# Optimization experiments

Measured on AMD Instinct MI355X. Metric: run time of the kernel, lower is better.

The kernel has to match this reference:

```python
import jax, jax.numpy as jnp
import numpy as np

N, F, E, WID, M, K = 100000, 128, 128, 4, 25000, 16
HID = WID * F    # width * num_features = 512
DHID = WID * E   # discriminator hidden = 512
EPS = 1e-5


def _v2v(x, v_idx, w_e):
    """Hypergraph v2v mean aggregation: v->e mean (scaled by w_e), then e->v mean."""
    Mm, Kk = v_idx.shape
    C = x.shape[1]
    ef = jnp.zeros((Mm, C), x.dtype)
    for k in range(Kk):  # K is small and static; avoids a [M,K,C] materialization
        ef = ef + x[v_idx[:, k]]
    ef = ef * (w_e / Kk)[:, None]  # weighted edge features [M, C]
    out = jnp.zeros_like(x)
    deg = jnp.zeros((x.shape[0],), x.dtype)
    for k in range(Kk):
        out = out.at[v_idx[:, k]].add(ef)
        deg = deg.at[v_idx[:, k]].add(1.0)
    return out / jnp.maximum(deg, 1.0)[:, None]


def _bn(h, g, bt):
    # BatchNorm1d in training mode: biased batch stats over vertex dim
    m = h.mean(0)
    v = ((h - m) ** 2).mean(0)
    return g * (h - m) * jax.lax.rsqrt(v + EPS) + bt


def _conv(x, Wt, b, g, bt, v_idx, w_e, last=False):
    h = _bn(x @ Wt.T + b, g, bt)
    h = _v2v(h, v_idx, w_e)
    return h if last else jax.nn.relu(h)  # dropout = identity (eval mode)


def setup_inputs() -> dict:
    key = jax.random.key(0)
    ks = iter(jax.random.split(key, 64))

    def lin(o, i):
        s = 1.0 / np.sqrt(i)
        return (jax.random.uniform(next(ks), (o, i), minval=-s, maxval=s, dtype=jnp.float32),
                jax.random.uniform(next(ks), (o,), minval=-s, maxval=s, dtype=jnp.float32))

    d = {}
    d["X"] = jax.random.normal(next(ks), (N, F), dtype=jnp.float32)
    d["v_idx"] = jax.random.randint(next(ks), (M, K), 0, N, dtype=jnp.int32)
    d["w_e"] = jax.random.uniform(next(ks), (M,), dtype=jnp.float32)
    for name, (o, i) in [("enc1", (HID, F)), ("enc2", (E, HID)), ("fc", (E, HID)),
                         ("f1u", (E, E)), ("f2u", (E, E)), ("f1r", (E, E)), ("f2r", (E, E)),
                         ("f1", (E, E)), ("f2", (E, E)),
                         ("dis1", (DHID, E)), ("dis2", (2, DHID)),
                         ("dec1", (HID, E)), ("dec2", (F, HID))]:
        Wt, b = lin(o, i)
        d[name + "_W"] = Wt
        d[name + "_b"] = b
    for name, c in [("enc1", HID), ("enc2", E), ("dis1", DHID), ("dis2", 2), ("dec1", HID), ("dec2", F)]:
        d[name + "_g"] = jnp.ones((c,), jnp.float32)
        d[name + "_bt"] = jnp.zeros((c,), jnp.float32)
    return d


def reference(X, v_idx, w_e,
              enc1_W, enc1_b, enc2_W, enc2_b, fc_W, fc_b,
              f1u_W, f1u_b, f2u_W, f2u_b, f1r_W, f1r_b, f2r_W, f2r_b,
              f1_W, f1_b, f2_W, f2_b,
              dis1_W, dis1_b, dis2_W, dis2_b, dec1_W, dec1_b, dec2_W, dec2_b,
              enc1_g, enc1_bt, enc2_g, enc2_bt, dis1_g, dis1_bt, dis2_g, dis2_bt,
              dec1_g, dec1_bt, dec2_g, dec2_bt):
    # encoder (returns last output and first-layer output)
    x1 = _conv(X, enc1_W, enc1_b, enc1_g, enc1_bt, v_idx, w_e)            # [N, HID]
    xe = _conv(x1, enc2_W, enc2_b, enc2_g, enc2_bt, v_idx, w_e, last=True)  # [N, E]
    xe1 = x1 @ fc_W.T + fc_b                                               # [N, E]
    # GRU-style gating
    z = jax.nn.sigmoid(xe1 @ f1u_W.T + f1u_b + xe @ f2u_W.T + f2u_b)
    r = jax.nn.sigmoid(xe1 @ f1r_W.T + f1r_b + xe @ f2r_W.T + f2r_b)
    o = jnp.tanh(xe1 @ f1_W.T + f1_b + (r * xe) @ f2_W.T + f2_b)
    outs = z * o + (1.0 - z) * xe                                          # [N, E]
    # attention pooling (n = input_size - 1)
    dd = (outs - outs.mean(0)) ** 2
    vv = dd.sum(0) / (N - 1)
    ee = dd / (4.0 * (vv + 0.001)) + 0.5
    proto = (outs * jax.nn.sigmoid(ee)).sum(0)                             # [E]
    # gradient reversal is identity in the forward pass
    h = _conv(outs, dis1_W, dis1_b, dis1_g, dis1_bt, v_idx, w_e)
    xdis = _conv(h, dis2_W, dis2_b, dis2_g, dis2_bt, v_idx, w_e, last=True)  # [N, 2]
    h = _conv(outs, dec1_W, dec1_b, dec1_g, dec1_bt, v_idx, w_e)
    x_de = _conv(h, dec2_W, dec2_b, dec2_g, dec2_bt, v_idx, w_e, last=True)  # [N, F]
    return (outs, x_de, proto, xdis)
```

## Files before the change

### kernel.cpp

```cpp
#include <hip/hip_runtime.h>
#include <cstddef>
#include <cstdint>

static constexpr int NV = 100000;
static constexpr int NP = 100096;
static constexpr int ME = 25000;
static constexpr int MEP = 25088;
static constexpr int KE = 16;
static constexpr float BN_EPS = 1e-5f;

typedef unsigned int u32;
typedef __attribute__((ext_vector_type(8))) short s16x8;
typedef __attribute__((ext_vector_type(8))) unsigned short u16x8;
typedef __attribute__((ext_vector_type(4))) float f32x4;

__device__ __forceinline__ float sigm(float x) { return 1.0f / (1.0f + expf(-x)); }
__device__ __forceinline__ float bf2f(unsigned short u) {
    union { u32 i; float f; } v; v.i = ((u32)u) << 16; return v.f;
}
__device__ __forceinline__ unsigned short f2bf(float f) {
    union { float f; u32 i; } v; v.f = f;
    u32 u = v.i;
    return (unsigned short)((u + 0x7FFFu + ((u >> 16) & 1u)) >> 16);
}

#define GLD16(g, l) __builtin_amdgcn_global_load_lds(                          \
    (__attribute__((address_space(1))) const unsigned int*)(g),                \
    (__attribute__((address_space(3))) unsigned int*)(l), 16, 0, 0)

__global__ __launch_bounds__(256)
void mfma_gemm(const unsigned short* __restrict__ A, int IC,
               const unsigned short* __restrict__ W, const float* __restrict__ bias,
               unsigned short* __restrict__ Cb, int ldb, int cb0,
               unsigned short* __restrict__ Cb2, int ldb2, int splitN,
               float* __restrict__ s1f, float* __restrict__ s2f, int statsC)
{
    __shared__ unsigned short smA[128 * 64];
    const int bm = blockIdx.y * 128;
    const int bn = blockIdx.x * 64;
    const int tid = threadIdx.x;
    const int l = tid & 63, w = tid >> 6;
    const int wrow = w >> 1, wcol = w & 1;

    f32x4 acc[4][2];
    #pragma unroll
    for (int m = 0; m < 4; ++m)
        #pragma unroll
        for (int n = 0; n < 2; ++n)
            #pragma unroll
            for (int r = 0; r < 4; ++r) acc[m][n][r] = 0.f;

    const int swz = (((l & 7) ^ (l >> 3)) << 3);

    for (int k0 = 0; k0 < IC; k0 += 64) {
        #pragma unroll
        for (int i = 0; i < 4; ++i) {
            const unsigned short* g = A + (size_t)(bm + 32 * w + 8 * i + (l >> 3)) * IC + k0 + swz;
            GLD16(g, smA + 2048 * w + 512 * i);
        }
        s16x8 bfr[2][2];
        #pragma unroll
        for (int n = 0; n < 2; ++n)
            #pragma unroll
            for (int ks = 0; ks < 2; ++ks) {
                int col = bn + wcol * 32 + n * 16 + (l & 15);
                bfr[n][ks] = *(const s16x8*)&W[(size_t)col * IC + k0 + ks * 32 + ((l >> 4) << 3)];
            }
        __syncthreads();
        #pragma unroll
        for (int ks = 0; ks < 2; ++ks) {
            s16x8 afr[4];
            #pragma unroll
            for (int m = 0; m < 4; ++m) {
                int row = wrow * 64 + m * 16 + (l & 15);
                int off = row * 64 + ((ks * 32 + ((l >> 4) << 3)) ^ ((l & 7) << 3));
                afr[m] = *(const s16x8*)&smA[off];
            }
            #pragma unroll
            for (int m = 0; m < 4; ++m)
                #pragma unroll
                for (int n = 0; n < 2; ++n)
                    acc[m][n] = __builtin_amdgcn_mfma_f32_16x16x32_bf16(
                        afr[m], bfr[n][ks], acc[m][n], 0, 0, 0);
        }
        __syncthreads();
    }

    unsigned short* dst = Cb;
    int ld = ldb, co = cb0;
    if (Cb2 && bn >= splitN) { dst = Cb2; ld = ldb2; co = -splitN; }

    #pragma unroll
    for (int n = 0; n < 2; ++n) {
        const int col = bn + wcol * 32 + n * 16 + (l & 15);
        const float bs = bias[col];
        float ssum = 0.f, sq = 0.f;
        #pragma unroll
        for (int m = 0; m < 4; ++m) {
            const int row0 = bm + wrow * 64 + m * 16 + ((l >> 4) << 2);
            #pragma unroll
            for (int r = 0; r < 4; ++r) {
                float v = acc[m][n][r] + bs;
                int row = row0 + r;
                if (dst) dst[(size_t)row * ld + co + col] = f2bf(v);
                if (s1f && col < statsC && row < NV) { ssum += v; sq += v * v; }
            }
        }
        if (s1f && col < statsC) {
            ssum += __shfl_xor(ssum, 16); ssum += __shfl_xor(ssum, 32);
            sq   += __shfl_xor(sq, 16);   sq   += __shfl_xor(sq, 32);
            if ((l >> 4) == 0) {
                atomicAdd(&s1f[col], ssum);
                atomicAdd(&s2f[col], sq);
            }
        }
    }
}

__global__ __launch_bounds__(256)
void mfma_gemm_ef(const unsigned short* __restrict__ A,
                  const unsigned short* __restrict__ W,
                  const float* __restrict__ we,
                  const float* __restrict__ P, const float* __restrict__ Q,
                  unsigned short* __restrict__ ef, int ldE)
{
    __shared__ unsigned short smA[128 * 64];
    const int bm = blockIdx.y * 128;
    const int bn = blockIdx.x * 64;
    const int tid = threadIdx.x;
    const int l = tid & 63, w = tid >> 6;
    const int wrow = w >> 1, wcol = w & 1;

    f32x4 acc[4][2];
    #pragma unroll
    for (int m = 0; m < 4; ++m)
        #pragma unroll
        for (int n = 0; n < 2; ++n)
            #pragma unroll
            for (int r = 0; r < 4; ++r) acc[m][n][r] = 0.f;

    const int swz = (((l & 7) ^ (l >> 3)) << 3);

    for (int k0 = 0; k0 < 128; k0 += 64) {
        #pragma unroll
        for (int i = 0; i < 4; ++i) {
            const unsigned short* g = A + (size_t)(bm + 32 * w + 8 * i + (l >> 3)) * 128 + k0 + swz;
            GLD16(g, smA + 2048 * w + 512 * i);
        }
        s16x8 bfr[2][2];
        #pragma unroll
        for (int n = 0; n < 2; ++n)
            #pragma unroll
            for (int ks = 0; ks < 2; ++ks) {
                int col = bn + wcol * 32 + n * 16 + (l & 15);
                bfr[n][ks] = *(const s16x8*)&W[(size_t)col * 128 + k0 + ks * 32 + ((l >> 4) << 3)];
            }
        __syncthreads();
        #pragma unroll
        for (int ks = 0; ks < 2; ++ks) {
            s16x8 afr[4];
            #pragma unroll
            for (int m = 0; m < 4; ++m) {
                int row = wrow * 64 + m * 16 + (l & 15);
                int off = row * 64 + ((ks * 32 + ((l >> 4) << 3)) ^ ((l & 7) << 3));
                afr[m] = *(const s16x8*)&smA[off];
            }
            #pragma unroll
            for (int m = 0; m < 4; ++m)
                #pragma unroll
                for (int n = 0; n < 2; ++n)
                    acc[m][n] = __builtin_amdgcn_mfma_f32_16x16x32_bf16(
                        afr[m], bfr[n][ks], acc[m][n], 0, 0, 0);
        }
        __syncthreads();
    }

    #pragma unroll
    for (int n = 0; n < 2; ++n) {
        const int col = bn + wcol * 32 + n * 16 + (l & 15);
        const float pc = P[col], qc = Q[col];
        #pragma unroll
        for (int m = 0; m < 4; ++m) {
            const int row0 = bm + wrow * 64 + m * 16 + ((l >> 4) << 2);
            #pragma unroll
            for (int r = 0; r < 4; ++r) {
                int row = row0 + r;
                if (row < ME) {
                    float wv = we[row];
                    ef[(size_t)row * ldE + col] = f2bf(wv * (pc * acc[m][n][r] + qc));
                }
            }
        }
    }
}

__global__ void prep_weights(const float* e1, const float* e2, const float* fcw,
                             const float* d1, const float* dc1, const float* dc2,
                             const float* ds2,
                             const float* f1u, const float* f2u,
                             const float* f1r, const float* f2r,
                             const float* f1, const float* f2,
                             const float* f1ub, const float* f2ub,
                             const float* f1rb, const float* f2rb,
                             const float* f1b, const float* f2b,
                             const float* ds1b, const float* dc1b,
                             const float* e2b, const float* fcb,
                             unsigned short* WB, float* bzr, float* bo,
                             float* bdd, float* bef)
{
    int i = blockIdx.x * 256 + threadIdx.x;
    if (i < 65536)           WB[i] = f2bf(e1[i]);
    else if (i < 131072)     WB[i] = f2bf(e2[i - 65536]);
    else if (i < 196608)     WB[i] = f2bf(fcw[i - 131072]);
    else if (i < 262144)     WB[i] = f2bf(d1[i - 196608]);
    else if (i < 327680)     WB[i] = f2bf(dc1[i - 262144]);
    else if (i < 393216)     WB[i] = f2bf(dc2[i - 327680]);
    else if (i < 394240)     WB[i] = f2bf(ds2[i - 393216]);
    else if (i < 459776) {
        int j = i - 394240, row = j >> 8, c = j & 255;
        float v;
        if (row < 128) v = (c < 128) ? f1u[row * 128 + c] : f2u[row * 128 + c - 128];
        else { int rr = row - 128; v = (c < 128) ? f1r[rr * 128 + c] : f2r[rr * 128 + c - 128]; }
        WB[i] = f2bf(v);
    } else if (i < 492544) {
        int j = i - 459776, row = j >> 8, c = j & 255;
        float v = (c < 128) ? f1[row * 128 + c] : f2[row * 128 + c - 128];
        WB[i] = f2bf(v);
    } else if (i < 492800) {
        int o = i - 492544;
        bzr[o] = (o < 128) ? (f1ub[o] + f2ub[o]) : (f1rb[o - 128] + f2rb[o - 128]);
    } else if (i < 492928) {
        int o = i - 492800;
        bo[o] = f1b[o] + f2b[o];
    } else if (i < 493952) {
        int o = i - 492928;
        bdd[o] = (o < 512) ? ds1b[o] : dc1b[o - 512];
    } else if (i < 494208) {
        int o = i - 493952;
        bef[o] = (o < 128) ? e2b[o] : fcb[o - 128];
    }
}

__global__ void cvt_f32_bf16(const float* __restrict__ in, unsigned short* __restrict__ out, int n)
{
    int i = (blockIdx.x * 256 + threadIdx.x) * 4;
    if (i < n) {
        float4 v = *reinterpret_cast<const float4*>(&in[i]);
        out[i] = f2bf(v.x); out[i + 1] = f2bf(v.y);
        out[i + 2] = f2bf(v.z); out[i + 3] = f2bf(v.w);
    }
}

__global__ void bn_finalize_kernel(const float* __restrict__ s1, const float* __restrict__ s2,
                                   const float* __restrict__ g, const float* __restrict__ bt,
                                   float* __restrict__ scale, float* __restrict__ shift,
                                   int C, float invN)
{
    int c = threadIdx.x;
    if (c < C) {
        float m = s1[c] * invN;
        float v = fmaxf(s2[c] * invN - m * m, 0.f);
        float sc = g[c] * rsqrtf(v + BN_EPS);
        scale[c] = sc;
        shift[c] = bt[c] - m * sc;
    }
}

__global__ void bn_finalize_pq(const float* __restrict__ s1, const float* __restrict__ s2,
                               const float* __restrict__ g, const float* __restrict__ bt,
                               const float* __restrict__ bias,
                               float* __restrict__ P, float* __restrict__ Q,
                               int C, int off, float invN)
{
    int c = threadIdx.x;
    if (c < C) {
        int cc = off + c;
        float m = s1[cc] * invN;
        float v = fmaxf(s2[cc] * invN - m * m, 0.f);
        float sc = g[c] * rsqrtf(v + BN_EPS);
        float sh = bt[c] - m * sc;
        P[cc] = sc * (1.0f / KE);
        Q[cc] = sc * bias[c] + sh;
    }
}

__global__ __launch_bounds__(256)
void edge_gather_sum(const unsigned short* __restrict__ x, const int* __restrict__ vidx,
                     unsigned short* __restrict__ ge)
{
    const int e = blockIdx.x * 16 + (threadIdx.x >> 4);
    const int cp = (threadIdx.x & 15) << 3;
    if (e >= ME) return;
    float s[8] = {};
    const int* vi = vidx + e * KE;
    #pragma unroll
    for (int k = 0; k < KE; ++k) {
        int v = vi[k];
        u16x8 u = *(const u16x8*)&x[(size_t)v * 128 + cp];
        #pragma unroll
        for (int j = 0; j < 8; ++j) s[j] += bf2f(u[j]);
    }
    u16x8 o;
    #pragma unroll
    for (int j = 0; j < 8; ++j) o[j] = f2bf(s[j]);
    *(u16x8*)&ge[(size_t)e * 128 + cp] = o;
}

__global__ __launch_bounds__(256)
void edge_gather_bf(const unsigned short* __restrict__ pre, const int* __restrict__ vidx,
                    const float* __restrict__ we, const float* __restrict__ scl,
                    const float* __restrict__ shf, unsigned short* __restrict__ ef, int C)
{
    const int tpe = C >> 3;
    const int epb = 256 / tpe;
    const int e = blockIdx.x * epb + threadIdx.x / tpe;
    const int cp = (threadIdx.x % tpe) << 3;
    if (e >= ME) return;
    float s[8] = {};
    const int* vi = vidx + e * KE;
    #pragma unroll
    for (int k = 0; k < KE; ++k) {
        int v = vi[k];
        u16x8 u = *(const u16x8*)&pre[(size_t)v * C + cp];
        #pragma unroll
        for (int j = 0; j < 8; ++j) s[j] += bf2f(u[j]);
    }
    float wv = we[e] * (1.0f / KE);
    u16x8 o;
    #pragma unroll
    for (int j = 0; j < 8; ++j)
        o[j] = f2bf(wv * (scl[cp + j] * s[j] + (float)KE * shf[cp + j]));
    *(u16x8*)&ef[(size_t)e * C + cp] = o;
}

__global__ void edge_gather2_kernel(const float* __restrict__ X, const int* __restrict__ vidx,
                                    const float* __restrict__ we, const float* __restrict__ scale,
                                    const float* __restrict__ shift, float* __restrict__ ef)
{
    int e = blockIdx.x * blockDim.x + threadIdx.x;
    if (e >= ME) return;
    float s0 = 0.f, s1v = 0.f;
    #pragma unroll
    for (int k = 0; k < KE; ++k) {
        int v = vidx[e * KE + k];
        s0 += X[2 * v];
        s1v += X[2 * v + 1];
    }
    float w = we[e] * (1.0f / KE);
    ef[2 * e]     = w * (scale[0] * s0 + (float)KE * shift[0]);
    ef[2 * e + 1] = w * (scale[1] * s1v + (float)KE * shift[1]);
}

__global__ void deg_kernel(const int* __restrict__ vidx, int* __restrict__ deg)
{
    int i = blockIdx.x * blockDim.x + threadIdx.x;
    if (i < ME * KE) atomicAdd(&deg[vidx[i]], 1);
}

__global__ void scan_block_kernel(const int* __restrict__ deg, int* __restrict__ rowptr,
                                  int* __restrict__ blocksums, int n)
{
    __shared__ int tmp[256];
    int i = blockIdx.x * 256 + threadIdx.x;
    int v = (i < n) ? deg[i] : 0;
    tmp[threadIdx.x] = v;
    __syncthreads();
    for (int off = 1; off < 256; off <<= 1) {
        int t = (threadIdx.x >= off) ? tmp[threadIdx.x - off] : 0;
        __syncthreads();
        tmp[threadIdx.x] += t;
        __syncthreads();
    }
    if (i < n) rowptr[i] = tmp[threadIdx.x] - v;
    if (threadIdx.x == 255) blocksums[blockIdx.x] = tmp[255];
}

__global__ void scan_sums_par(int* __restrict__ bs, int nb)
{
    __shared__ int tmp[512];
    int t = threadIdx.x;
    int v = (t < nb) ? bs[t] : 0;
    tmp[t] = v;
    __syncthreads();
    for (int off = 1; off < 512; off <<= 1) {
        int u = (t >= off) ? tmp[t - off] : 0;
        __syncthreads();
        tmp[t] += u;
        __syncthreads();
    }
    if (t < nb) bs[t] = tmp[t] - v;
}

__global__ void scan_add_kernel(int* __restrict__ rowptr, const int* __restrict__ blocksums, int n)
{
    int i = blockIdx.x * 256 + threadIdx.x;
    if (i < n) rowptr[i] += blocksums[blockIdx.x];
    if (i == 0) rowptr[n] = ME * KE;
}

__global__ void csr_fill_kernel(const int* __restrict__ vidx, int* __restrict__ cursor,
                                int* __restrict__ csr)
{
    int i = blockIdx.x * blockDim.x + threadIdx.x;
    if (i < ME * KE) {
        int v = vidx[i];
        int pos = atomicAdd(&cursor[v], 1);
        csr[pos] = i >> 4;
    }
}

__global__ __launch_bounds__(256)
void csr_gather_bf(const unsigned short* __restrict__ ef, int ldE, int cb0E,
                   const int* __restrict__ rowptr, const int* __restrict__ csr,
                   float* __restrict__ outf, int ldf,
                   unsigned short* __restrict__ outb, int ldb, int cb0,
                   unsigned short* __restrict__ outb2, int ldb2,
                   int C, int relu)
{
    const int lpv = C >> 3;
    const int vpb = 256 / lpv;
    const int v = blockIdx.x * vpb + threadIdx.x / lpv;
    const int lg = threadIdx.x % lpv;
    if (v >= NV) return;
    const int s = rowptr[v], e = rowptr[v + 1];
    float a[8] = {};
    int i = s;
    for (; i + 2 <= e; i += 2) {
        int e0 = csr[i], e1 = csr[i + 1];
        u16x8 u0 = *(const u16x8*)&ef[(size_t)e0 * ldE + cb0E + lg * 8];
        u16x8 u1 = *(const u16x8*)&ef[(size_t)e1 * ldE + cb0E + lg * 8];
        #pragma unroll
        for (int j = 0; j < 8; ++j) a[j] += bf2f(u0[j]) + bf2f(u1[j]);
    }
    if (i < e) {
        int e0 = csr[i];
        u16x8 u0 = *(const u16x8*)&ef[(size_t)e0 * ldE + cb0E + lg * 8];
        #pragma unroll
        for (int j = 0; j < 8; ++j) a[j] += bf2f(u0[j]);
    }
    float inv = 1.0f / (float)max(e - s, 1);
    #pragma unroll
    for (int j = 0; j < 8; ++j) {
        float x = a[j] * inv;
        if (relu) x = fmaxf(x, 0.f);
        a[j] = x;
    }
    if (outf) {
        float* p = outf + (size_t)v * ldf + lg * 8;
        #pragma unroll
        for (int j = 0; j < 8; ++j) p[j] = a[j];
    }
    if (outb) {
        u16x8 o;
        #pragma unroll
        for (int j = 0; j < 8; ++j) o[j] = f2bf(a[j]);
        *(u16x8*)&outb[(size_t)v * ldb + cb0 + lg * 8] = o;
    }
    if (outb2) {
        u16x8 o;
        #pragma unroll
        for (int j = 0; j < 8; ++j) o[j] = f2bf(a[j]);
        *(u16x8*)&outb2[(size_t)v * ldb2 + lg * 8] = o;
    }
}

__global__ void csr_gather2_kernel(const float* __restrict__ ef, const int* __restrict__ rowptr,
                                   const int* __restrict__ csr, float* __restrict__ outp)
{
    int v = blockIdx.x * blockDim.x + threadIdx.x;
    if (v >= NV) return;
    int s = rowptr[v], e = rowptr[v + 1];
    float a0 = 0.f, a1 = 0.f;
    for (int i = s; i < e; ++i) {
        int ed = csr[i];
        a0 += ef[2 * ed];
        a1 += ef[2 * ed + 1];
    }
    float inv = 1.0f / (float)max(e - s, 1);
    outp[2 * v]     = a0 * inv;
    outp[2 * v + 1] = a1 * inv;
}

__global__ __launch_bounds__(256)
void dis2_dot(const unsigned short* __restrict__ A, const unsigned short* __restrict__ Wd,
              const float* __restrict__ bias, float* __restrict__ pre)
{
    const int wid = threadIdx.x >> 6, l = threadIdx.x & 63;
    const int v = blockIdx.x * 4 + wid;
    if (v >= NV) return;
    u16x8 a = *(const u16x8*)&A[(size_t)v * 512 + l * 8];
    u16x8 w0 = *(const u16x8*)&Wd[l * 8];
    u16x8 w1 = *(const u16x8*)&Wd[512 + l * 8];
    float d0 = 0.f, d1 = 0.f;
    #pragma unroll
    for (int j = 0; j < 8; ++j) {
        float av = bf2f(a[j]);
        d0 += av * bf2f(w0[j]);
        d1 += av * bf2f(w1[j]);
    }
    for (int o = 32; o > 0; o >>= 1) {
        d0 += __shfl_down(d0, o);
        d1 += __shfl_down(d1, o);
    }
    if (l == 0) {
        pre[2 * v]     = d0 + bias[0];
        pre[2 * v + 1] = d1 + bias[1];
    }
}

__global__ __launch_bounds__(256)
void colstats_bf(const unsigned short* __restrict__ Xb,
                 float* __restrict__ s1, float* __restrict__ s2)
{
    const int t = threadIdx.x;
    const int cg = t & 15;
    const int rs = t >> 4;
    float s[8] = {}, q[8] = {};
    for (int r = blockIdx.x * 16 + rs; r < NV; r += 256 * 16) {
        u16x8 u = *(const u16x8*)&Xb[(size_t)r * 128 + cg * 8];
        #pragma unroll
        for (int j = 0; j < 8; ++j) {
            float v = bf2f(u[j]);
            s[j] += v; q[j] += v * v;
        }
    }
    __shared__ float ls[16][16][8];
    __shared__ float lq[16][16][8];
    #pragma unroll
    for (int j = 0; j < 8; ++j) { ls[rs][cg][j] = s[j]; lq[rs][cg][j] = q[j]; }
    __syncthreads();
    int c = t & 127;
    float a = 0.f;
    if (t < 128) {
        #pragma unroll
        for (int i = 0; i < 16; ++i) a += ls[i][c >> 3][c & 7];
        atomicAdd(&s1[c], a);
    } else {
        #pragma unroll
        for (int i = 0; i < 16; ++i) a += lq[i][c >> 3][c & 7];
        atomicAdd(&s2[c], a);
    }
}

__global__ void att_finalize_kernel(const float* __restrict__ s1, const float* __restrict__ s2,
                                    float* __restrict__ mu, float* __restrict__ qd, int C)
{
    int c = threadIdx.x;
    if (c < C) {
        float m = s1[c] / (float)NV;
        float vv = fmaxf((s2[c] - (float)NV * m * m) / (float)(NV - 1), 0.f);
        mu[c] = m;
        qd[c] = 1.0f / (4.0f * (vv + 0.001f));
    }
}

__global__ __launch_bounds__(256)
void proto_ws(const float* __restrict__ outsf, const float* __restrict__ mu,
              const float* __restrict__ qd, float* __restrict__ proto)
{
    const int t = threadIdx.x;
    const int cg = t & 31;
    const int rs = t >> 5;
    const float4* X4 = (const float4*)outsf;
    const float4 m = ((const float4*)mu)[cg];
    const float4 q = ((const float4*)qd)[cg];
    float4 acc = make_float4(0.f, 0.f, 0.f, 0.f);
    for (int r = blockIdx.x * 8 + rs; r < NV; r += 256 * 8) {
        float4 x = X4[(size_t)r * 32 + cg];
        float d0 = (x.x - m.x) * (x.x - m.x);
        float d1 = (x.y - m.y) * (x.y - m.y);
        float d2 = (x.z - m.z) * (x.z - m.z);
        float d3 = (x.w - m.w) * (x.w - m.w);
        acc.x += x.x * sigm(d0 * q.x + 0.5f);
        acc.y += x.y * sigm(d1 * q.y + 0.5f);
        acc.z += x.z * sigm(d2 * q.z + 0.5f);
        acc.w += x.w * sigm(d3 * q.w + 0.5f);
    }
    __shared__ float4 ls[8][32];
    ls[rs][cg] = acc;
    __syncthreads();
    if (t < 128) {
        float a = 0.f;
        #pragma unroll
        for (int i = 0; i < 8; ++i) {
            const float* f = (const float*)&ls[i][t >> 2];
            a += f[t & 3];
        }
        atomicAdd(&proto[t], a);
    }
}

__global__ void colstats2_kernel(const float* __restrict__ X, int N,
                                 float* __restrict__ s1, float* __restrict__ s2)
{
    __shared__ float red[256][4];
    int t = threadIdx.x;
    float a0 = 0, a1 = 0, b0 = 0, b1 = 0;
    for (int r = blockIdx.x * 256 + t; r < N; r += 256 * gridDim.x) {
        float x0 = X[2 * r], x1 = X[2 * r + 1];
        a0 += x0; b0 += x0 * x0;
        a1 += x1; b1 += x1 * x1;
    }
    red[t][0] = a0; red[t][1] = a1; red[t][2] = b0; red[t][3] = b1;
    __syncthreads();
    for (int s = 128; s > 0; s >>= 1) {
        if (t < s)
            for (int j = 0; j < 4; ++j) red[t][j] += red[t + s][j];
        __syncthreads();
    }
    if (t == 0) {
        atomicAdd(&s1[0], red[0][0]);
        atomicAdd(&s1[1], red[0][1]);
        atomicAdd(&s2[0], red[0][2]);
        atomicAdd(&s2[1], red[0][3]);
    }
}

__global__ void rx_kernel(const unsigned short* __restrict__ ZR, const unsigned short* __restrict__ xeb,
                          unsigned short* __restrict__ G, int n8)
{
    int idx = blockIdx.x * blockDim.x + threadIdx.x;
    if (idx >= n8) return;
    int i8 = idx * 8;
    int row = i8 >> 7, c = i8 & 127;
    u16x8 rv = *(const u16x8*)&ZR[(size_t)row * 256 + 128 + c];
    u16x8 xv = *(const u16x8*)&xeb[i8];
    u16x8 g;
    #pragma unroll
    for (int j = 0; j < 8; ++j)
        g[j] = f2bf(sigm(bf2f(rv[j])) * bf2f(xv[j]));
    *(u16x8*)&G[(size_t)row * 256 + 128 + c] = g;
}

__global__ void gru_out_kernel(const unsigned short* __restrict__ ZR, const unsigned short* __restrict__ Opre,
                               const unsigned short* __restrict__ xeb,
                               float* __restrict__ outs, unsigned short* __restrict__ outsb,
                               float* __restrict__ outsf, int n8)
{
    int idx = blockIdx.x * blockDim.x + threadIdx.x;
    if (idx >= n8) return;
    int i8 = idx * 8;
    int row = i8 >> 7, c = i8 & 127;
    u16x8 zv = *(const u16x8*)&ZR[(size_t)row * 256 + c];
    u16x8 ov = *(const u16x8*)&Opre[i8];
    u16x8 xv = *(const u16x8*)&xeb[i8];
    float val[8];
    u16x8 ob;
    #pragma unroll
    for (int j = 0; j < 8; ++j) {
        float z = sigm(bf2f(zv[j]));
        float o = tanhf(bf2f(ov[j]));
        float xe = bf2f(xv[j]);
        val[j] = z * o + (1.f - z) * xe;
        ob[j] = f2bf(val[j]);
    }
    *(float4*)&outs[i8]     = make_float4(val[0], val[1], val[2], val[3]);
    *(float4*)&outs[i8 + 4] = make_float4(val[4], val[5], val[6], val[7]);
    *(float4*)&outsf[i8]     = make_float4(val[0], val[1], val[2], val[3]);
    *(float4*)&outsf[i8 + 4] = make_float4(val[4], val[5], val[6], val[7]);
    *(u16x8*)&outsb[i8] = ob;
}

extern "C" void kernel_launch(void* const* d_in, const int* in_sizes, int n_in,
                              void* d_out, int out_size, void* d_ws, size_t ws_size,
                              hipStream_t stream)
{
    const float* X      = (const float*)d_in[0];
    const int*   vidx   = (const int*)  d_in[1];
    const float* we     = (const float*)d_in[2];
    const float* enc1_W = (const float*)d_in[3];  const float* enc1_b = (const float*)d_in[4];
    const float* enc2_W = (const float*)d_in[5];  const float* enc2_b = (const float*)d_in[6];
    const float* fc_W   = (const float*)d_in[7];  const float* fc_b   = (const float*)d_in[8];
    const float* f1u_W  = (const float*)d_in[9];  const float* f1u_b  = (const float*)d_in[10];
    const float* f2u_W  = (const float*)d_in[11]; const float* f2u_b  = (const float*)d_in[12];
    const float* f1r_W  = (const float*)d_in[13]; const float* f1r_b  = (const float*)d_in[14];
    const float* f2r_W  = (const float*)d_in[15]; const float* f2r_b  = (const float*)d_in[16];
    const float* f1_W   = (const float*)d_in[17]; const float* f1_b   = (const float*)d_in[18];
    const float* f2_W   = (const float*)d_in[19]; const float* f2_b   = (const float*)d_in[20];
    const float* dis1_W = (const float*)d_in[21]; const float* dis1_b = (const float*)d_in[22];
    const float* dis2_W = (const float*)d_in[23]; const float* dis2_b = (const float*)d_in[24];
    const float* dec1_W = (const float*)d_in[25]; const float* dec1_b = (const float*)d_in[26];
    const float* dec2_W = (const float*)d_in[27]; const float* dec2_b = (const float*)d_in[28];
    const float* enc1_g = (const float*)d_in[29]; const float* enc1_bt = (const float*)d_in[30];
    const float* enc2_g = (const float*)d_in[31]; const float* enc2_bt = (const float*)d_in[32];
    const float* dis1_g = (const float*)d_in[33]; const float* dis1_bt = (const float*)d_in[34];
    const float* dis2_g = (const float*)d_in[35]; const float* dis2_bt = (const float*)d_in[36];
    const float* dec1_g = (const float*)d_in[37]; const float* dec1_bt = (const float*)d_in[38];
    const float* dec2_g = (const float*)d_in[39]; const float* dec2_bt = (const float*)d_in[40];

    float* out   = (float*)d_out;
    float* outs  = out;
    float* x_de  = out + 12800000;
    float* proto = out + 25600000;
    float* xdis  = out + 25600128;

    char* base = (char*)d_ws;
    unsigned short* bufA = (unsigned short*)base;
    char* p = base + (size_t)NP * 512 * 2;
    unsigned short* bufE = (unsigned short*)p; p += (size_t)MEP * 1024 * 2;
    unsigned short* Greg = (unsigned short*)p;
    unsigned short* Xbf  = Greg;
    unsigned short* outsb = Greg + (size_t)NP * 128;
    p += (size_t)NP * 256 * 2;
    unsigned short* x1bf = (unsigned short*)p; p += (size_t)NP * 512 * 2;
    unsigned short* WB = (unsigned short*)p; p += 492544 * 2 + 1024;
    float* bzr = (float*)p; p += 256 * 4;
    float* bo  = (float*)p; p += 128 * 4;
    float* bdd = (float*)p; p += 1024 * 4;
    float* bef = (float*)p; p += 256 * 4;
    float* s1  = (float*)p; p += 1024 * 4;
    float* s2  = (float*)p; p += 1024 * 4;
    float* scl = (float*)p; p += 1024 * 4;
    float* shf = (float*)p; p += 1024 * 4;
    int* deg    = (int*)p; p += (size_t)NV * 4;
    int* rowptr = (int*)p; p += (size_t)(NV + 1) * 4;
    int* cursor = (int*)p; p += (size_t)NV * 4;
    int* bsums  = (int*)p; p += 512 * 4;
    int* csr    = (int*)p; p += (size_t)ME * KE * 4;
    float* outsf = (float*)p; p += (size_t)NP * 128 * 4;
    unsigned short* ge = (unsigned short*)p;

    unsigned short* pre128 = bufA;
    unsigned short* xe_bf  = bufA + (size_t)NP * 128;
    unsigned short* ZR     = bufA + (size_t)NP * 256;
    unsigned short* Opre   = bufA;
    unsigned short* hdec   = bufA;
    float* pre22 = (float*)(Greg + (size_t)NP * 128);
    float* bufEf = (float*)bufE;

    unsigned short* wenc1 = WB;
    unsigned short* wenc2 = WB + 65536;
    unsigned short* wdd   = WB + 196608;
    unsigned short* wdec2 = WB + 327680;
    unsigned short* wdis2 = WB + 393216;
    unsigned short* wzr   = WB + 394240;
    unsigned short* wo    = WB + 459776;

    const int n128 = NV * 128;
    const int n8 = n128 / 8;
    const int nScanBlocks = (NV + 255) / 256;

    auto gemm = [&](const unsigned short* A, int ic, const unsigned short* W, const float* b,
                    unsigned short* Cb, int ldb, int cb0,
                    unsigned short* Cb2, int ldb2, int splitN,
                    int oc, float* st1, float* st2, int statsC) {
        dim3 g(oc / 64, NP / 128);
        mfma_gemm<<<g, 256, 0, stream>>>(A, ic, W, b, Cb, ldb, cb0, Cb2, ldb2, splitN,
                                         st1, st2, statsC);
    };

    prep_weights<<<1931, 256, 0, stream>>>(enc1_W, enc2_W, fc_W, dis1_W, dec1_W, dec2_W, dis2_W,
                                           f1u_W, f2u_W, f1r_W, f2r_W, f1_W, f2_W,
                                           f1u_b, f2u_b, f1r_b, f2r_b, f1_b, f2_b,
                                           dis1_b, dec1_b, enc2_b, fc_b,
                                           WB, bzr, bo, bdd, bef);
    cvt_f32_bf16<<<(n128 / 4 + 255) / 256, 256, 0, stream>>>(X, Xbf, n128);

    hipMemsetAsync(deg, 0, NV * sizeof(int), stream);
    deg_kernel<<<(ME * KE + 255) / 256, 256, 0, stream>>>(vidx, deg);
    scan_block_kernel<<<nScanBlocks, 256, 0, stream>>>(deg, rowptr, bsums, NV);
    scan_sums_par<<<1, 512, 0, stream>>>(bsums, nScanBlocks);
    scan_add_kernel<<<nScanBlocks, 256, 0, stream>>>(rowptr, bsums, NV);
    hipMemcpyAsync(cursor, rowptr, NV * sizeof(int), hipMemcpyDeviceToDevice, stream);
    csr_fill_kernel<<<(ME * KE + 255) / 256, 256, 0, stream>>>(vidx, cursor, csr);

    hipMemsetAsync(s1, 0, 2048 * sizeof(float), stream);
    gemm(Xbf, 128, wenc1, enc1_b, nullptr, 0, 0, nullptr, 0, 1 << 30, 512, s1, s2, 512);
    bn_finalize_pq<<<1, 512, 0, stream>>>(s1, s2, enc1_g, enc1_bt, enc1_b, scl, shf, 512, 0, 1.0f / NV);
    edge_gather_sum<<<(ME + 15) / 16, 256, 0, stream>>>(Xbf, vidx, ge);
    { dim3 g(8, MEP / 128);
      mfma_gemm_ef<<<g, 256, 0, stream>>>(ge, wenc1, we, scl, shf, bufE, 512); }
    csr_gather_bf<<<NV / 4, 256, 0, stream>>>(bufE, 512, 0, rowptr, csr,
        nullptr, 0, x1bf, 512, 0, nullptr, 0, 512, 1);

    hipMemsetAsync(s1, 0, 2048 * sizeof(float), stream);
    gemm(x1bf, 512, wenc2, bef, pre128, 128, 0, Greg, 256, 128, 256, s1, s2, 128);
    bn_finalize_kernel<<<1, 512, 0, stream>>>(s1, s2, enc2_g, enc2_bt, scl, shf, 128, 1.0f / NV);
    edge_gather_bf<<<(ME + 15) / 16, 256, 0, stream>>>(pre128, vidx, we, scl, shf, bufE, 128);
    csr_gather_bf<<<NV / 16, 256, 0, stream>>>(bufE, 128, 0, rowptr, csr,
        nullptr, 0, Greg, 256, 128, xe_bf, 128, 128, 0);

    gemm(Greg, 256, wzr, bzr, ZR, 256, 0, nullptr, 0, 1 << 30, 256, nullptr, nullptr, 0);
    rx_kernel<<<(n8 + 255) / 256, 256, 0, stream>>>(ZR, xe_bf, Greg, n8);
    gemm(Greg, 256, wo, bo, Opre, 128, 0, nullptr, 0, 1 << 30, 128, nullptr, nullptr, 0);
    gru_out_kernel<<<(n8 + 255) / 256, 256, 0, stream>>>(ZR, Opre, xe_bf, outs, outsb, outsf, n8);

    hipMemsetAsync(s1, 0, 2048 * sizeof(float), stream);
    colstats_bf<<<256, 256, 0, stream>>>(outsb, s1, s2);
    att_finalize_kernel<<<1, 128, 0, stream>>>(s1, s2, scl, shf, 128);
    hipMemsetAsync(proto, 0, 128 * sizeof(float), stream);
    proto_ws<<<256, 256, 0, stream>>>(outsf, scl, shf, proto);

    hipMemsetAsync(s1, 0, 2048 * sizeof(float), stream);
    gemm(outsb, 128, wdd, bdd, nullptr, 0, 0, nullptr, 0, 1 << 30, 1024, s1, s2, 1024);
    bn_finalize_pq<<<1, 512, 0, stream>>>(s1, s2, dis1_g, dis1_bt, dis1_b, scl, shf, 512, 0, 1.0f / NV);
    bn_finalize_pq<<<1, 512, 0, stream>>>(s1, s2, dec1_g, dec1_bt, dec1_b, scl, shf, 512, 512, 1.0f / NV);
    edge_gather_sum<<<(ME + 15) / 16, 256, 0, stream>>>(outsb, vidx, ge);
    { dim3 g(16, MEP / 128);
      mfma_gemm_ef<<<g, 256, 0, stream>>>(ge, wdd, we, scl, shf, bufE, 1024); }
    csr_gather_bf<<<NV / 4, 256, 0, stream>>>(bufE, 1024, 0, rowptr, csr,
        nullptr, 0, x1bf, 512, 0, nullptr, 0, 512, 1);
    csr_gather_bf<<<NV / 4, 256, 0, stream>>>(bufE, 1024, 512, rowptr, csr,
        nullptr, 0, hdec, 512, 0, nullptr, 0, 512, 1);

    dis2_dot<<<NV / 4, 256, 0, stream>>>(x1bf, wdis2, dis2_b, pre22);
    hipMemsetAsync(s1, 0, 2048 * sizeof(float), stream);
    colstats2_kernel<<<64, 256, 0, stream>>>(pre22, NV, s1, s2);
    bn_finalize_kernel<<<1, 512, 0, stream>>>(s1, s2, dis2_g, dis2_bt, scl, shf, 2, 1.0f / NV);
    edge_gather2_kernel<<<(ME + 255) / 256, 256, 0, stream>>>(pre22, vidx, we, scl, shf, bufEf);
    csr_gather2_kernel<<<(NV + 255) / 256, 256, 0, stream>>>(bufEf, rowptr, csr, xdis);

    hipMemsetAsync(s1, 0, 2048 * sizeof(float), stream);
    gemm(hdec, 512, wdec2, dec2_b, Greg, 128, 0, nullptr, 0, 1 << 30, 128, s1, s2, 128);
    bn_finalize_kernel<<<1, 512, 0, stream>>>(s1, s2, dec2_g, dec2_bt, scl, shf, 128, 1.0f / NV);
    edge_gather_bf<<<(ME + 15) / 16, 256, 0, stream>>>(Greg, vidx, we, scl, shf, bufE, 128);
    csr_gather_bf<<<NV / 16, 256, 0, stream>>>(bufE, 128, 0, rowptr, csr,
        x_de, 128, nullptr, 0, 0, nullptr, 0, 128, 0);
}
```

Before: 975.5 us.

## Derive BN stats from input covariance, double-buffer GEMM tiles, fuse dis2 gather

Replaces the full N×512 and N×1024 GEMMs that existed only to compute batch-norm column sums and squares with an input covariance (X^T X via MFMA) plus a per-output-column quadratic form. This removes a large GEMM pass and its output stats atomics. The GEMM kernels now double-buffer both A and W tiles in LDS with async loads, so the next tile's load overlaps the current MFMAs. The two dis/dec CSR gathers and the dis2 dot product are merged into one kernel, which avoids writing and rereading x1bf. A risk is precision: second moments computed as E[x^2] from a bf16 covariance may suffer cancellation.

After: 901.1 us. 7.6% less time.

```diff
diff --git a/kernel.cpp b/kernel.cpp
--- a/kernel.cpp
+++ b/kernel.cpp
@@ -28,6 +28,22 @@
     (__attribute__((address_space(1))) const unsigned int*)(g),                \
     (__attribute__((address_space(3))) unsigned int*)(l), 16, 0, 0)
 
+#define STAGE_AB(b, k0)                                                        \
+  {                                                                            \
+    unsigned short* sA_ = sm + (b) * 12288;                                    \
+    unsigned short* sB_ = sA_ + 8192;                                          \
+    _Pragma("unroll")                                                          \
+    for (int i_ = 0; i_ < 4; ++i_) {                                           \
+      const unsigned short* g_ = A + (size_t)(bm + 32 * w + 8 * i_ + (l >> 3)) * IC + (k0) + swz; \
+      GLD16(g_, sA_ + 2048 * w + 512 * i_);                                    \
+    }                                                                          \
+    _Pragma("unroll")                                                          \
+    for (int i_ = 0; i_ < 2; ++i_) {                                           \
+      const unsigned short* g_ = W + (size_t)(bn + 16 * w + 8 * i_ + (l >> 3)) * IC + (k0) + swz; \
+      GLD16(g_, sB_ + 1024 * w + 512 * i_);                                    \
+    }                                                                          \
+  }
+
 __global__ __launch_bounds__(256)
 void mfma_gemm(const unsigned short* __restrict__ A, int IC,
                const unsigned short* __restrict__ W, const float* __restrict__ bias,
@@ -35,7 +51,7 @@
                unsigned short* __restrict__ Cb2, int ldb2, int splitN,
                float* __restrict__ s1f, float* __restrict__ s2f, int statsC)
 {
-    __shared__ unsigned short smA[128 * 64];
+    __shared__ unsigned short sm[2 * 12288];
     const int bm = blockIdx.y * 128;
     const int bn = blockIdx.x * 64;
     const int tid = threadIdx.x;
@@ -51,39 +67,40 @@
             for (int r = 0; r < 4; ++r) acc[m][n][r] = 0.f;
 
     const int swz = (((l & 7) ^ (l >> 3)) << 3);
-
-    for (int k0 = 0; k0 < IC; k0 += 64) {
-        #pragma unroll
-        for (int i = 0; i < 4; ++i) {
-            const unsigned short* g = A + (size_t)(bm + 32 * w + 8 * i + (l >> 3)) * IC + k0 + swz;
-            GLD16(g, smA + 2048 * w + 512 * i);
-        }
-        s16x8 bfr[2][2];
-        #pragma unroll
-        for (int n = 0; n < 2; ++n)
-            #pragma unroll
-            for (int ks = 0; ks < 2; ++ks) {
-                int col = bn + wcol * 32 + n * 16 + (l & 15);
-                bfr[n][ks] = *(const s16x8*)&W[(size_t)col * IC + k0 + ks * 32 + ((l >> 4) << 3)];
-            }
-        __syncthreads();
+    const int nt = IC >> 6;
+
+    STAGE_AB(0, 0);
+    asm volatile("s_waitcnt vmcnt(0)" ::: "memory");
+    __builtin_amdgcn_s_barrier();
+
+    for (int t = 0; t < nt; ++t) {
+        const int cur = t & 1;
+        if (t + 1 < nt) STAGE_AB(cur ^ 1, (t + 1) << 6);
+        const unsigned short* sA = sm + cur * 12288;
+        const unsigned short* sB = sA + 8192;
         #pragma unroll
         for (int ks = 0; ks < 2; ++ks) {
-            s16x8 afr[4];
+            const int koff = ks * 32 + ((l >> 4) << 3);
+            s16x8 afr[4], bfr[2];
             #pragma unroll
             for (int m = 0; m < 4; ++m) {
                 int row = wrow * 64 + m * 16 + (l & 15);
-                int off = row * 64 + ((ks * 32 + ((l >> 4) << 3)) ^ ((l & 7) << 3));
-                afr[m] = *(const s16x8*)&smA[off];
+                afr[m] = *(const s16x8*)&sA[row * 64 + (koff ^ ((l & 7) << 3))];
+            }
+            #pragma unroll
+            for (int n = 0; n < 2; ++n) {
+                int col = wcol * 32 + n * 16 + (l & 15);
+                bfr[n] = *(const s16x8*)&sB[col * 64 + (koff ^ ((l & 7) << 3))];
             }
             #pragma unroll
             for (int m = 0; m < 4; ++m)
                 #pragma unroll
                 for (int n = 0; n < 2; ++n)
                     acc[m][n] = __builtin_amdgcn_mfma_f32_16x16x32_bf16(
-                        afr[m], bfr[n][ks], acc[m][n], 0, 0, 0);
-        }
-        __syncthreads();
+                        afr[m], bfr[n], acc[m][n], 0, 0, 0);
+        }
+        asm volatile("s_waitcnt vmcnt(0)" ::: "memory");
+        __builtin_amdgcn_s_barrier();
     }
 
     unsigned short* dst = Cb;
@@ -124,7 +141,8 @@
                   const float* __restrict__ P, const float* __restrict__ Q,
                   unsigned short* __restrict__ ef, int ldE)
 {
-    __shared__ unsigned short smA[128 * 64];
+    const int IC = 128;
+    __shared__ unsigned short sm[2 * 12288];
     const int bm = blockIdx.y * 128;
     const int bn = blockIdx.x * 64;
     const int tid = threadIdx.x;
@@ -141,38 +159,39 @@
 
     const int swz = (((l & 7) ^ (l >> 3)) << 3);
 
-    for (int k0 = 0; k0 < 128; k0 += 64) {
-        #pragma unroll
-        for (int i = 0; i < 4; ++i) {
-            const unsigned short* g = A + (size_t)(bm + 32 * w + 8 * i + (l >> 3)) * 128 + k0 + swz;
-            GLD16(g, smA + 2048 * w + 512 * i);
-        }
-        s16x8 bfr[2][2];
-        #pragma unroll
-        for (int n = 0; n < 2; ++n)
-            #pragma unroll
-            for (int ks = 0; ks < 2; ++ks) {
-                int col = bn + wcol * 32 + n * 16 + (l & 15);
-                bfr[n][ks] = *(const s16x8*)&W[(size_t)col * 128 + k0 + ks * 32 + ((l >> 4) << 3)];
-            }
-        __syncthreads();
+    STAGE_AB(0, 0);
+    asm volatile("s_waitcnt vmcnt(0)" ::: "memory");
+    __builtin_amdgcn_s_barrier();
+
+    #pragma unroll
+    for (int t = 0; t < 2; ++t) {
+        const int cur = t & 1;
+        if (t == 0) STAGE_AB(1, 64);
+        const unsigned short* sA = sm + cur * 12288;
+        const unsigned short* sB = sA + 8192;
         #pragma unroll
         for (int ks = 0; ks < 2; ++ks) {
-            s16x8 afr[4];
+            const int koff = ks * 32 + ((l >> 4) << 3);
+            s16x8 afr[4], bfr[2];
             #pragma unroll
             for (int m = 0; m < 4; ++m) {
                 int row = wrow * 64 + m * 16 + (l & 15);
-                int off = row * 64 + ((ks * 32 + ((l >> 4) << 3)) ^ ((l & 7) << 3));
-                afr[m] = *(const s16x8*)&smA[off];
+                afr[m] = *(const s16x8*)&sA[row * 64 + (koff ^ ((l & 7) << 3))];
+            }
+            #pragma unroll
+            for (int n = 0; n < 2; ++n) {
+                int col = wcol * 32 + n * 16 + (l & 15);
+                bfr[n] = *(const s16x8*)&sB[col * 64 + (koff ^ ((l & 7) << 3))];
             }
             #pragma unroll
             for (int m = 0; m < 4; ++m)
                 #pragma unroll
                 for (int n = 0; n < 2; ++n)
                     acc[m][n] = __builtin_amdgcn_mfma_f32_16x16x32_bf16(
-                        afr[m], bfr[n][ks], acc[m][n], 0, 0, 0);
-        }
-        __syncthreads();
+                        afr[m], bfr[n], acc[m][n], 0, 0, 0);
+        }
+        asm volatile("s_waitcnt vmcnt(0)" ::: "memory");
+        __builtin_amdgcn_s_barrier();
     }
 
     #pragma unroll
@@ -191,6 +210,105 @@
                 }
             }
         }
+    }
+}
+
+__global__ __launch_bounds__(256)
+void cov_kernel(const unsigned short* __restrict__ A, float* __restrict__ cov)
+{
+    __shared__ unsigned short T[128 * 64];
+    const int tid = threadIdx.x;
+    const int l = tid & 63, w = tid >> 6;
+
+    f32x4 acc[2][8];
+    #pragma unroll
+    for (int m = 0; m < 2; ++m)
+        #pragma unroll
+        for (int n = 0; n < 8; ++n)
+            #pragma unroll
+            for (int r = 0; r < 4; ++r) acc[m][n][r] = 0.f;
+
+    const int r0 = blockIdx.x * 1024;
+    for (int ch = 0; ch < 16; ++ch) {
+        const int rbase = r0 + ch * 64;
+        __syncthreads();
+        #pragma unroll
+        for (int q = 0; q < 4; ++q) {
+            int idx = tid + q * 256;
+            int r = idx & 63, cg = idx >> 6;
+            int row = rbase + r;
+            u16x8 u = {0, 0, 0, 0, 0, 0, 0, 0};
+            if (row < NV) u = *(const u16x8*)&A[(size_t)row * 128 + cg * 8];
+            #pragma unroll
+            for (int j = 0; j < 8; ++j) {
+                int c = cg * 8 + j;
+                T[c * 64 + (r ^ ((c & 7) << 3))] = u[j];
+            }
+        }
+        __syncthreads();
+        #pragma unroll
+        for (int ks = 0; ks < 2; ++ks) {
+            const int koff = ks * 32 + ((l >> 4) << 3);
+            s16x8 fi[2], fj[8];
+            #pragma unroll
+            for (int m = 0; m < 2; ++m) {
+                int c = (w * 2 + m) * 16 + (l & 15);
+                fi[m] = *(const s16x8*)&T[c * 64 + (koff ^ ((c & 7) << 3))];
+            }
+            #pragma unroll
+            for (int n = 0; n < 8; ++n) {
+                int c = n * 16 + (l & 15);
+                fj[n] = *(const s16x8*)&T[c * 64 + (koff ^ ((c & 7) << 3))];
+            }
+            #pragma unroll
+            for (int m = 0; m < 2; ++m)
+                #pragma unroll
+                for (int n = 0; n < 8; ++n)
+                    acc[m][n] = __builtin_amdgcn_mfma_f32_16x16x32_bf16(
+                        fi[m], fj[n], acc[m][n], 0, 0, 0);
+        }
+    }
+    #pragma unroll
+    for (int m = 0; m < 2; ++m) {
+        #pragma unroll
+        for (int n = 0; n < 8; ++n) {
+            #pragma unroll
+            for (int r = 0; r < 4; ++r) {
+                int row = (w * 2 + m) * 16 + ((l >> 4) << 2) + r;
+                int col = n * 16 + (l & 15);
+                atomicAdd(&cov[row * 128 + col], acc[m][n][r]);
+            }
+        }
+    }
+}
+
+__global__ __launch_bounds__(128)
+void quadform_kernel(const float* __restrict__ cov, const float* __restrict__ colsum,
+                     const unsigned short* __restrict__ Wt, const float* __restrict__ bias,
+                     float* __restrict__ s1, float* __restrict__ s2)
+{
+    const int c = blockIdx.x, i = threadIdx.x;
+    __shared__ float wv[128];
+    __shared__ float red[128][2];
+    float wi = bf2f(Wt[c * 128 + i]);
+    wv[i] = wi;
+    __syncthreads();
+    const float* crow = cov + i * 128;
+    float dot = 0.f;
+    #pragma unroll 8
+    for (int j = 0; j < 128; ++j) dot += crow[j] * wv[j];
+    red[i][0] = wi * dot;
+    red[i][1] = wi * colsum[i];
+    __syncthreads();
+    for (int s = 64; s > 0; s >>= 1) {
+        if (i < s) { red[i][0] += red[i + s][0]; red[i][1] += red[i + s][1]; }
+        __syncthreads();
+    }
+    if (i == 0) {
+        float b = bias[c];
+        float ws = red[0][1];
+        s1[c] = ws + (float)NV * b;
+        s2[c] = red[0][0] + 2.f * b * ws + (float)NV * b * b;
     }
 }
 
@@ -464,6 +582,60 @@
     }
 }
 
+__global__ __launch_bounds__(256)
+void csr_gather_dd(const unsigned short* __restrict__ ef,
+                   const int* __restrict__ rowptr, const int* __restrict__ csr,
+                   const unsigned short* __restrict__ wdis2, const float* __restrict__ dis2b,
+                   float* __restrict__ pre22, unsigned short* __restrict__ hdec)
+{
+    const int w = threadIdx.x >> 6, l = threadIdx.x & 63;
+    const int v = blockIdx.x * 2 + (w >> 1);
+    const int half = w & 1;
+    const int s = rowptr[v], e = rowptr[v + 1];
+    const int cp = half * 512 + l * 8;
+    float a[8] = {};
+    int i = s;
+    for (; i + 2 <= e; i += 2) {
+        int e0 = csr[i], e1 = csr[i + 1];
+        u16x8 u0 = *(const u16x8*)&ef[(size_t)e0 * 1024 + cp];
+        u16x8 u1 = *(const u16x8*)&ef[(size_t)e1 * 1024 + cp];
+        #pragma unroll
+        for (int j = 0; j < 8; ++j) a[j] += bf2f(u0[j]) + bf2f(u1[j]);
+    }
+    if (i < e) {
+        int e0 = csr[i];
+        u16x8 u0 = *(const u16x8*)&ef[(size_t)e0 * 1024 + cp];
+        #pragma unroll
+        for (int j = 0; j < 8; ++j) a[j] += bf2f(u0[j]);
+    }
+    float inv = 1.0f / (float)max(e - s, 1);
+    #pragma unroll
+    for (int j = 0; j < 8; ++j) a[j] = fmaxf(a[j] * inv, 0.f);
+    if (half == 0) {
+        u16x8 w0 = *(const u16x8*)&wdis2[l * 8];
+        u16x8 w1 = *(const u16x8*)&wdis2[512 + l * 8];
+        float d0 = 0.f, d1 = 0.f;
+        #pragma unroll
+        for (int j = 0; j < 8; ++j) {
+            d0 += a[j] * bf2f(w0[j]);
+            d1 += a[j] * bf2f(w1[j]);
+        }
+        for (int o = 32; o > 0; o >>= 1) {
+            d0 += __shfl_down(d0, o);
+            d1 += __shfl_down(d1, o);
+        }
+        if (l == 0) {
+            pre22[2 * v]     = d0 + dis2b[0];
+            pre22[2 * v + 1] = d1 + dis2b[1];
+        }
+    } else {
+        u16x8 o8;
+        #pragma unroll
+        for (int j = 0; j < 8; ++j) o8[j] = f2bf(a[j]);
+        *(u16x8*)&hdec[(size_t)v * 512 + l * 8] = o8;
+    }
+}
+
 __global__ void csr_gather2_kernel(const float* __restrict__ ef, const int* __restrict__ rowptr,
                                    const int* __restrict__ csr, float* __restrict__ outp)
 {
@@ -479,33 +651,6 @@
     float inv = 1.0f / (float)max(e - s, 1);
     outp[2 * v]     = a0 * inv;
     outp[2 * v + 1] = a1 * inv;
-}
-
-__global__ __launch_bounds__(256)
-void dis2_dot(const unsigned short* __restrict__ A, const unsigned short* __restrict__ Wd,
-              const float* __restrict__ bias, float* __restrict__ pre)
-{
-    const int wid = threadIdx.x >> 6, l = threadIdx.x & 63;
-    const int v = blockIdx.x * 4 + wid;
-    if (v >= NV) return;
-    u16x8 a = *(const u16x8*)&A[(size_t)v * 512 + l * 8];
-    u16x8 w0 = *(const u16x8*)&Wd[l * 8];
-    u16x8 w1 = *(const u16x8*)&Wd[512 + l * 8];
-    float d0 = 0.f, d1 = 0.f;
-    #pragma unroll
-    for (int j = 0; j < 8; ++j) {
-        float av = bf2f(a[j]);
-        d0 += av * bf2f(w0[j]);
-        d1 += av * bf2f(w1[j]);
-    }
-    for (int o = 32; o > 0; o >>= 1) {
-        d0 += __shfl_down(d0, o);
-        d1 += __shfl_down(d1, o);
-    }
-    if (l == 0) {
-        pre[2 * v]     = d0 + bias[0];
-        pre[2 * v + 1] = d1 + bias[1];
-    }
 }
 
 __global__ __launch_bounds__(256)
@@ -712,6 +857,12 @@
     float* s2  = (float*)p; p += 1024 * 4;
     float* scl = (float*)p; p += 1024 * 4;
     float* shf = (float*)p; p += 1024 * 4;
+    float* sX1 = (float*)p; p += 128 * 4;
+    float* sX2 = (float*)p; p += 128 * 4;
+    float* sA1 = (float*)p; p += 128 * 4;
+    float* sA2 = (float*)p; p += 128 * 4;
+    float* covX = (float*)p; p += 16384 * 4;
+    float* covA = (float*)p; p += 16384 * 4;
     int* deg    = (int*)p; p += (size_t)NV * 4;
     int* rowptr = (int*)p; p += (size_t)(NV + 1) * 4;
     int* cursor = (int*)p; p += (size_t)NV * 4;
@@ -764,8 +915,11 @@
     hipMemcpyAsync(cursor, rowptr, NV * sizeof(int), hipMemcpyDeviceToDevice, stream);
     csr_fill_kernel<<<(ME * KE + 255) / 256, 256, 0, stream>>>(vidx, cursor, csr);
 
-    hipMemsetAsync(s1, 0, 2048 * sizeof(float), stream);
-    gemm(Xbf, 128, wenc1, enc1_b, nullptr, 0, 0, nullptr, 0, 1 << 30, 512, s1, s2, 512);
+    hipMemsetAsync(sX1, 0, 256 * sizeof(float), stream);
+    hipMemsetAsync(covX, 0, 16384 * sizeof(float), stream);
+    colstats_bf<<<256, 256, 0, stream>>>(Xbf, sX1, sX2);
+    cov_kernel<<<98, 256, 0, stream>>>(Xbf, covX);
+    quadform_kernel<<<512, 128, 0, stream>>>(covX, sX1, wenc1, enc1_b, s1, s2);
     bn_finalize_pq<<<1, 512, 0, stream>>>(s1, s2, enc1_g, enc1_bt, enc1_b, scl, shf, 512, 0, 1.0f / NV);
     edge_gather_sum<<<(ME + 15) / 16, 256, 0, stream>>>(Xbf, vidx, ge);
     { dim3 g(8, MEP / 128);
@@ -785,25 +939,22 @@
     gemm(Greg, 256, wo, bo, Opre, 128, 0, nullptr, 0, 1 << 30, 128, nullptr, nullptr, 0);
     gru_out_kernel<<<(n8 + 255) / 256, 256, 0, stream>>>(ZR, Opre, xe_bf, outs, outsb, outsf, n8);
 
-    hipMemsetAsync(s1, 0, 2048 * sizeof(float), stream);
-    colstats_bf<<<256, 256, 0, stream>>>(outsb, s1, s2);
-    att_finalize_kernel<<<1, 128, 0, stream>>>(s1, s2, scl, shf, 128);
+    hipMemsetAsync(sA1, 0, 256 * sizeof(float), stream);
+    colstats_bf<<<256, 256, 0, stream>>>(outsb, sA1, sA2);
+    att_finalize_kernel<<<1, 128, 0, stream>>>(sA1, sA2, scl, shf, 128);
     hipMemsetAsync(proto, 0, 128 * sizeof(float), stream);
     proto_ws<<<256, 256, 0, stream>>>(outsf, scl, shf, proto);
 
-    hipMemsetAsync(s1, 0, 2048 * sizeof(float), stream);
-    gemm(outsb, 128, wdd, bdd, nullptr, 0, 0, nullptr, 0, 1 << 30, 1024, s1, s2, 1024);
+    hipMemsetAsync(covA, 0, 16384 * sizeof(float), stream);
+    cov_kernel<<<98, 256, 0, stream>>>(outsb, covA);
+    quadform_kernel<<<1024, 128, 0, stream>>>(covA, sA1, wdd, bdd, s1, s2);
     bn_finalize_pq<<<1, 512, 0, stream>>>(s1, s2, dis1_g, dis1_bt, dis1_b, scl, shf, 512, 0, 1.0f / NV);
     bn_finalize_pq<<<1, 512, 0, stream>>>(s1, s2, dec1_g, dec1_bt, dec1_b, scl, shf, 512, 512, 1.0f / NV);
     edge_gather_sum<<<(ME + 15) / 16, 256, 0, stream>>>(outsb, vidx, ge);
     { dim3 g(16, MEP / 128);
       mfma_gemm_ef<<<g, 256, 0, stream>>>(ge, wdd, we, scl, shf, bufE, 1024); }
-    csr_gather_bf<<<NV / 4, 256, 0, stream>>>(bufE, 1024, 0, rowptr, csr,
-        nullptr, 0, x1bf, 512, 0, nullptr, 0, 512, 1);
-    csr_gather_bf<<<NV / 4, 256, 0, stream>>>(bufE, 1024, 512, rowptr, csr,
-        nullptr, 0, hdec, 512, 0, nullptr, 0, 512, 1);
-
-    dis2_dot<<<NV / 4, 256, 0, stream>>>(x1bf, wdis2, dis2_b, pre22);
+    csr_gather_dd<<<NV / 2, 256, 0, stream>>>(bufE, rowptr, csr, wdis2, dis2_b, pre22, hdec);
+
     hipMemsetAsync(s1, 0, 2048 * sizeof(float), stream);
     colstats2_kernel<<<64, 256, 0, stream>>>(pre22, NV, s1, s2);
     bn_finalize_kernel<<<1, 512, 0, stream>>>(s1, s2, dis2_g, dis2_bt, scl, shf, 2, 1.0f / NV);
```
